# Kernel tuning notes

Measured on AMD Instinct MI355X. Metric: run time of the kernel, lower is better.

The kernel has to match this reference:

```python
import jax, jax.numpy as jnp
import numpy as np

HEADS = 8


def setup_inputs() -> dict:
    key = jax.random.key(0)
    ks = jax.random.split(key, 18)
    B, L, D, N = 512, 70, 128, 100000
    r = lambda i, shape: jax.random.normal(ks[i], shape, dtype=jnp.float32) * 0.1
    return {
        "hidden": r(0, (B, L, D)),
        "hidden0": r(1, (B, L, D)),
        "mask": jnp.ones((B, L), dtype=jnp.int32),
        "s": r(2, (B, D)),
        "emb": r(3, (N, D)),
        "attn_in_w": r(4, (3 * D, D)),
        "attn_in_b": r(5, (3 * D,)),
        "attn_out_w": r(6, (D, D)),
        "attn_out_b": r(7, (D,)),
        "w_zero": r(8, (D, D)),
        "b_zero": r(9, (D,)),
        "w_one": r(10, (D, D)),
        "b_one": r(11, (D,)),
        "w_two": r(12, (D, D)),
        "b_two": r(13, (D,)),
        "w_three": r(14, (HEADS, D)),
        "w_gate": r(15, (1, 2 * D)),
        "w_trans": r(16, (D, 2 * D)),
        "b_trans": r(17, (D,)),
    }


def _mha(q, k, v, in_w, in_b, out_w, out_b, h):
    # torch.nn.MultiheadAttention, eval mode (dropout=0)
    B, Lq, D = q.shape
    Lk = k.shape[1]
    hd = D // h
    wq, wk, wv = jnp.split(in_w, 3, axis=0)
    bq, bk, bv = jnp.split(in_b, 3)
    qp = (q @ wq.T + bq).reshape(B, Lq, h, hd)
    kp = (k @ wk.T + bk).reshape(B, Lk, h, hd)
    vp = (v @ wv.T + bv).reshape(B, Lk, h, hd)
    scores = jnp.einsum("bqhd,bkhd->bhqk", qp, kp) / jnp.sqrt(jnp.float32(hd))
    w = jax.nn.softmax(scores, axis=-1)
    o = jnp.einsum("bhqk,bkhd->bqhd", w, vp).reshape(B, Lq, D)
    return o @ out_w.T + out_b


def reference(hidden, hidden0, mask, s, emb,
              attn_in_w, attn_in_b, attn_out_w, attn_out_b,
              w_zero, b_zero, w_one, b_one, w_two, b_two,
              w_three, w_gate, w_trans, b_trans):
    B, L, D = hidden.shape
    H = HEADS
    # last-item gather (last_k = 1)
    last_idx = jnp.clip(jnp.sum(mask, axis=1) - 1, 0, 1000)
    ht0 = hidden[jnp.arange(B), last_idx]  # [B, D]
    ht1 = ht0
    # attention of pooled session vector over item states
    ht = _mha(s[:, None, :], hidden, hidden,
              attn_in_w, attn_in_b, attn_out_w, attn_out_b, H)  # [B, 1, D]
    # sigmoid gated fusion of hidden0 / hidden
    sigma = jax.nn.sigmoid(jnp.concatenate([hidden0, hidden], axis=-1) @ w_gate.T)  # [B, L, 1]
    hidden = hidden0 * sigma + hidden * (1.0 - sigma)
    # additive multi-head attention scores
    q0 = (ht1 @ w_zero.T + b_zero)[:, None, :]          # [B, 1, D]
    q1 = ht @ w_one.T + b_one                           # [B, 1, D]
    q2 = hidden @ w_two.T + b_two                       # [B, L, D]
    alpha = jax.nn.sigmoid(q1 + q2 + q0) @ w_three.T    # [B, L, H]
    alpha = jnp.where((mask == 0)[:, :, None], -jnp.inf, alpha)
    alpha = jax.nn.softmax(alpha, axis=1)
    # head-split mask-weighted sum reduction
    mf = mask.astype(hidden.dtype)[:, :, None]
    a = jnp.sum((alpha[..., None] * hidden.reshape(B, L, H, D // H)).reshape(B, L, D) * mf, axis=1)  # [B, D]
    # hybrid transform with last item
    a = jnp.concatenate([a, ht0], axis=1) @ w_trans.T + b_trans
    # normalized scoring against item table (skipping padding idx 0)
    b = emb[1:]
    a = a / (jnp.linalg.norm(a, axis=1, keepdims=True) + 1e-12)
    b = b / (jnp.linalg.norm(b, axis=1, keepdims=True) + 1e-12)
    scores = 12.0 * (a @ b.T)  # [B, n_node-1]
    return scores
```

## Files before the change

kernel.cpp:

```cpp
#include <hip/hip_runtime.h>
#include <hip/hip_bf16.h>

#define B_SZ 512
#define L_SZ 70
#define D_SZ 128
#define NCOL 99999
#define M_ROWS (B_SZ * L_SZ)

typedef __attribute__((ext_vector_type(4))) float f32x4;
typedef __attribute__((ext_vector_type(8))) short bf16x8;
typedef __attribute__((ext_vector_type(4))) short s16x4;
typedef __attribute__((ext_vector_type(8))) unsigned short u16x8;

static __device__ __forceinline__ short f2bf(float x) {
    union { float f; unsigned u; } v; v.f = x;
    unsigned r = v.u + 0x7fffu + ((v.u >> 16) & 1u);
    return (short)(r >> 16);
}
static __device__ __forceinline__ float bf2f(unsigned short h) {
    union { unsigned u; float f; } v; v.u = ((unsigned)h) << 16; return v.f;
}

__global__ void k_prep(const float* attn_in_w, const float* w_two,
                       const float* attn_out_w, const float* w_zero,
                       const float* w_one, const float* w_trans,
                       short* Wkv, short* W2,
                       float* wqT, float* woT, float* w0T, float* w1T, float* wtT) {
    int i = blockIdx.x * 256 + threadIdx.x;
    if (i < 256 * 128) Wkv[i] = f2bf(attn_in_w[128 * 128 + i]);
    if (i < 128 * 128) {
        W2[i] = f2bf(w_two[i]);
        int r = i >> 7, c = i & 127;
        wqT[c * 128 + r] = attn_in_w[i];
        woT[c * 128 + r] = attn_out_w[i];
        w0T[c * 128 + r] = w_zero[i];
        w1T[c * 128 + r] = w_one[i];
    }
    if (i < 128 * 256) {
        int r = i >> 8, c = i & 255;
        wtT[c * 128 + r] = w_trans[i];
    }
}

__global__ void k_gatekv(const float* hidden, const float* hidden0, const float* w_gate,
                         const short* Wkv, const float* attn_in_b,
                         short* g_bf, short* kv) {
    __shared__ float wg[256];
    __shared__ short h_lds[64][136];
    int t = threadIdx.x;
    int r0 = blockIdx.x * 64;
    wg[t] = w_gate[t];
    int row = t >> 2, q = t & 3;
    const float* hrow  = hidden  + (size_t)(r0 + row) * 128;
    const float* h0row = hidden0 + (size_t)(r0 + row) * 128;
    float h[32], h0[32];
    for (int i = 0; i < 8; i++) {
        float4 a = *(const float4*)(hrow  + i * 16 + q * 4);
        float4 b = *(const float4*)(h0row + i * 16 + q * 4);
        h[i*4+0]=a.x; h[i*4+1]=a.y; h[i*4+2]=a.z; h[i*4+3]=a.w;
        h0[i*4+0]=b.x; h0[i*4+1]=b.y; h0[i*4+2]=b.z; h0[i*4+3]=b.w;
    }
    __syncthreads();
    float p = 0.f;
    for (int i = 0; i < 8; i++)
        for (int j = 0; j < 4; j++) {
            int c = i * 16 + q * 4 + j;
            p += h0[i*4+j] * wg[c] + h[i*4+j] * wg[128 + c];
        }
    p += __shfl_xor(p, 1);
    p += __shfl_xor(p, 2);
    float sg = 1.f / (1.f + __expf(-p));
    float om = 1.f - sg;
    for (int i = 0; i < 8; i++) {
        s16x4 gv, hv;
        for (int j = 0; j < 4; j++) {
            gv[j] = f2bf(h0[i*4+j] * sg + h[i*4+j] * om);
            hv[j] = f2bf(h[i*4+j]);
        }
        int c = i * 16 + q * 4;
        *(s16x4*)(g_bf + (size_t)(r0 + row) * 128 + c) = gv;
        *(s16x4*)(&h_lds[row][c]) = hv;
    }
    __syncthreads();
    int lane = t & 63, w = t >> 6;
    int arl = lane & 15, kg = lane >> 4;
    int kbase = kg * 8;
    bf16x8 aF[4];
    for (int kk = 0; kk < 4; kk++)
        aF[kk] = *(const bf16x8*)(&h_lds[w * 16 + arl][kbase + kk * 32]);
    int cl = lane & 15;
    int rowbase = r0 + w * 16 + kg * 4;
    for (int ct = 0; ct < 16; ct++) {
        int c = ct * 16 + cl;
        f32x4 acc = {0.f, 0.f, 0.f, 0.f};
        const short* Brow = Wkv + c * 128 + kbase;
        for (int kk = 0; kk < 4; kk++) {
            bf16x8 bF = *(const bf16x8*)(Brow + kk * 32);
            acc = __builtin_amdgcn_mfma_f32_16x16x32_bf16(aF[kk], bF, acc, 0, 0, 0);
        }
        float bias = attn_in_b[128 + c];
        for (int rg = 0; rg < 4; rg++)
            kv[(size_t)(rowbase + rg) * 256 + c] = f2bf(acc[rg] + bias);
    }
}

__global__ void k_attn(const float* hidden, const int* mask, const float* s,
                       const float* wqT, const float* attn_in_b,
                       const short* kv,
                       const float* woT, const float* attn_out_b,
                       const float* w0T, const float* b_zero,
                       const float* w1T, const float* b_one,
                       float* ht0, float* q01) {
    int b = blockIdx.x, t = threadIdx.x;
    __shared__ unsigned short kp_s[L_SZ][136];
    __shared__ float s_sh[128], qp_s[128], o_s[128], ht_s[128], ht0_s[128];
    __shared__ float sc[8][72];
    __shared__ int idx_sh;
    if (t < 64) {
        int acc = 0;
        for (int l = t; l < L_SZ; l += 64) acc += mask[b * L_SZ + l];
        for (int off = 32; off; off >>= 1) acc += __shfl_down(acc, off);
        if (t == 0) {
            int idx = acc - 1;
            if (idx < 0) idx = 0;
            if (idx > L_SZ - 1) idx = L_SZ - 1;
            idx_sh = idx;
        }
    }
    s_sh[t] = s[b * 128 + t];
    const unsigned short* kvrow = (const unsigned short*)kv + (size_t)b * L_SZ * 256;
    for (int i = t; i < L_SZ * 128; i += 128) {
        int l = i >> 7, d = i & 127;
        kp_s[l][d] = kvrow[l * 256 + d];
    }
    __syncthreads();
    {
        float h0 = hidden[((size_t)b * L_SZ + idx_sh) * 128 + t];
        ht0[b * 128 + t] = h0;
        ht0_s[t] = h0;
        float acc = attn_in_b[t];
        for (int k = 0; k < 128; k++) acc += s_sh[k] * wqT[k * 128 + t];
        qp_s[t] = acc;
    }
    __syncthreads();
    for (int task = t; task < 8 * L_SZ; task += 128) {
        int h = task / L_SZ, l = task - (task / L_SZ) * L_SZ;
        const u16x8* kp = (const u16x8*)&kp_s[l][h * 16];
        u16x8 k0 = kp[0], k1 = kp[1];
        float acc = 0.f;
        for (int j = 0; j < 8; j++)
            acc += qp_s[h * 16 + j] * bf2f(k0[j]) + qp_s[h * 16 + 8 + j] * bf2f(k1[j]);
        sc[h][l] = acc * 0.25f;
    }
    __syncthreads();
    if (t < 8) {
        float m = -1e30f;
        for (int l = 0; l < L_SZ; l++) m = fmaxf(m, sc[t][l]);
        float ssum = 0.f;
        for (int l = 0; l < L_SZ; l++) { float e = __expf(sc[t][l] - m); sc[t][l] = e; ssum += e; }
        float inv = 1.f / ssum;
        for (int l = 0; l < L_SZ; l++) sc[t][l] *= inv;
    }
    __syncthreads();
    {
        int h = t >> 4;
        float acc = 0.f;
        for (int l = 0; l < L_SZ; l++) acc += sc[h][l] * bf2f(kvrow[l * 256 + 128 + t]);
        o_s[t] = acc;
    }
    __syncthreads();
    {
        float acc = attn_out_b[t];
        for (int k = 0; k < 128; k++) acc += o_s[k] * woT[k * 128 + t];
        ht_s[t] = acc;
    }
    __syncthreads();
    {
        float acc = b_one[t] + b_zero[t];
        for (int k = 0; k < 128; k++) acc += ht_s[k] * w1T[k * 128 + t] + ht0_s[k] * w0T[k * 128 + t];
        q01[b * 128 + t] = acc;
    }
}

__global__ void k_gemm_q2_alpha(const short* g_bf, const short* W2, const float* b_two,
                                const float* q01, const float* w_three, float* alphaL) {
    int lane = threadIdx.x & 63, w = threadIdx.x >> 6;
    int r0 = blockIdx.x * 64 + w * 16;
    int ar = r0 + (lane & 15);
    int kbase = (lane >> 4) * 8;
    bf16x8 aF[4];
    const short* Arow = g_bf + ar * 128 + kbase;
    for (int kk = 0; kk < 4; kk++) aF[kk] = *(const bf16x8*)(Arow + kk * 32);
    float part[4][8];
    for (int r = 0; r < 4; r++)
        for (int h = 0; h < 8; h++) part[r][h] = 0.f;
    int cl = lane & 15;
    int rowbase = r0 + (lane >> 4) * 4;
    for (int ct = 0; ct < 8; ct++) {
        int c = ct * 16 + cl;
        f32x4 acc = {0.f, 0.f, 0.f, 0.f};
        const short* Brow = W2 + c * 128 + kbase;
        for (int kk = 0; kk < 4; kk++) {
            bf16x8 bF = *(const bf16x8*)(Brow + kk * 32);
            acc = __builtin_amdgcn_mfma_f32_16x16x32_bf16(aF[kk], bF, acc, 0, 0, 0);
        }
        float bias = b_two[c];
        for (int rg = 0; rg < 4; rg++) {
            int row = rowbase + rg;
            int bb = row / L_SZ;
            float val = acc[rg] + bias + q01[bb * 128 + c];
            float sg = 1.f / (1.f + __expf(-val));
            for (int h = 0; h < 8; h++) part[rg][h] += sg * w_three[h * 128 + c];
        }
    }
    for (int off = 1; off < 16; off <<= 1)
        for (int rg = 0; rg < 4; rg++)
            for (int h = 0; h < 8; h++)
                part[rg][h] += __shfl_xor(part[rg][h], off);
    if ((lane & 15) == 0) {
        for (int rg = 0; rg < 4; rg++) {
            int row = rowbase + rg;
            for (int h = 0; h < 8; h++) alphaL[row * 8 + h] = part[rg][h];
        }
    }
}

__global__ void k_alpha_a(const float* alphaL, const int* mask, const short* g_bf,
                          const float* ht0, const float* wtT, const float* b_trans,
                          short* a_bf) {
    int b = blockIdx.x, t = threadIdx.x;
    __shared__ float aw[L_SZ][8];
    __shared__ float mf[L_SZ];
    __shared__ float a_s[128];
    __shared__ float ht0_s[128];
    __shared__ float red[2];
    for (int i = t; i < L_SZ; i += 128) mf[i] = (float)mask[b * L_SZ + i];
    for (int i = t; i < L_SZ * 8; i += 128) aw[i >> 3][i & 7] = alphaL[b * L_SZ * 8 + i];
    ht0_s[t] = ht0[b * 128 + t];
    __syncthreads();
    if (t < 8) {
        float m = -1e30f;
        for (int l = 0; l < L_SZ; l++) {
            float v = (mf[l] == 0.f) ? -1e30f : aw[l][t];
            if (v > m) m = v;
        }
        float ssum = 0.f;
        for (int l = 0; l < L_SZ; l++) {
            float v = (mf[l] == 0.f) ? -1e30f : aw[l][t];
            float e = __expf(v - m);
            ssum += e; aw[l][t] = e;
        }
        float inv = 1.f / ssum;
        for (int l = 0; l < L_SZ; l++) aw[l][t] *= inv;
    }
    __syncthreads();
    int h = t >> 4;
    float acc = 0.f;
    const unsigned short* grow = (const unsigned short*)g_bf + b * L_SZ * 128 + t;
    for (int l = 0; l < L_SZ; l++) acc += aw[l][h] * bf2f(grow[l * 128]) * mf[l];
    a_s[t] = acc;
    __syncthreads();
    float a2 = b_trans[t];
    for (int k = 0; k < 128; k++)
        a2 += a_s[k] * wtT[k * 128 + t] + ht0_s[k] * wtT[(128 + k) * 128 + t];
    float sq = a2 * a2;
    for (int off = 32; off; off >>= 1) sq += __shfl_down(sq, off);
    if ((t & 63) == 0) red[t >> 6] = sq;
    __syncthreads();
    float nrm = sqrtf(red[0] + red[1]) + 1e-12f;
    a_bf[b * 128 + t] = f2bf(a2 / nrm);
}

__global__ void __launch_bounds__(256, 4) k_final(const short* a_bf, const float* emb, float* out) {
    __shared__ float cbuf[4][16][36];
    int t = threadIdx.x;
    int lane = t & 63, w = t >> 6;
    int bx = blockIdx.x;
    int cl = lane & 15, kg = lane >> 4;
    int kbase = kg * 8;

    bf16x8 bF[2][4];
    for (int ct2 = 0; ct2 < 2; ct2++) {
        int c0 = bx * 128 + w * 32 + ct2 * 16 + cl;
        float x[4][8];
        float ss = 0.f;
        if (c0 < NCOL) {
            const float* e = emb + (size_t)(c0 + 1) * 128 + kbase;
            for (int kk = 0; kk < 4; kk++) {
                float4 v0 = *(const float4*)(e + kk * 32);
                float4 v1 = *(const float4*)(e + kk * 32 + 4);
                x[kk][0] = v0.x; x[kk][1] = v0.y; x[kk][2] = v0.z; x[kk][3] = v0.w;
                x[kk][4] = v1.x; x[kk][5] = v1.y; x[kk][6] = v1.z; x[kk][7] = v1.w;
                for (int j = 0; j < 8; j++) ss += x[kk][j] * x[kk][j];
            }
        } else {
            for (int kk = 0; kk < 4; kk++)
                for (int j = 0; j < 8; j++) x[kk][j] = 0.f;
        }
        ss += __shfl_xor(ss, 16);
        ss += __shfl_xor(ss, 32);
        float inv = 1.f / (sqrtf(ss) + 1e-12f);
        for (int kk = 0; kk < 4; kk++) {
            bf16x8 f;
            for (int j = 0; j < 8; j++) f[j] = f2bf(x[kk][j] * inv);
            bF[ct2][kk] = f;
        }
    }

    int cend = NCOL - bx * 128;
    if (cend > 128) cend = 128;
    int srow = lane >> 2, schunk = lane & 3;
    int scb = w * 32 + schunk * 8;

    for (int rt = 0; rt < 32; rt++) {
        bf16x8 aF[4];
        const short* Arow = a_bf + (size_t)(rt * 16 + cl) * 128 + kbase;
        for (int kk = 0; kk < 4; kk++) aF[kk] = *(const bf16x8*)(Arow + kk * 32);
        f32x4 acc0 = {0.f, 0.f, 0.f, 0.f}, acc1 = {0.f, 0.f, 0.f, 0.f};
        for (int kk = 0; kk < 4; kk++) {
            acc0 = __builtin_amdgcn_mfma_f32_16x16x32_bf16(aF[kk], bF[0][kk], acc0, 0, 0, 0);
            acc1 = __builtin_amdgcn_mfma_f32_16x16x32_bf16(aF[kk], bF[1][kk], acc1, 0, 0, 0);
        }
        for (int rg = 0; rg < 4; rg++) {
            cbuf[w][kg * 4 + rg][cl]      = 12.f * acc0[rg];
            cbuf[w][kg * 4 + rg][16 + cl] = 12.f * acc1[rg];
        }
        asm volatile("s_waitcnt lgkmcnt(0)" ::: "memory");
        f32x4 v0 = *(const f32x4*)&cbuf[w][srow][schunk * 8];
        f32x4 v1 = *(const f32x4*)&cbuf[w][srow][schunk * 8 + 4];
        asm volatile("s_waitcnt lgkmcnt(0)" ::: "memory");
        size_t gr = (size_t)(rt * 16 + srow) * NCOL + (size_t)bx * 128 + scb;
        if (scb + 7 < cend) {
            *(f32x4*)(out + gr) = v0;
            *(f32x4*)(out + gr + 4) = v1;
        } else {
            for (int j = 0; j < 4; j++) if (scb + j < cend) out[gr + j] = v0[j];
            for (int j = 0; j < 4; j++) if (scb + 4 + j < cend) out[gr + 4 + j] = v1[j];
        }
    }
}

extern "C" void kernel_launch(void* const* d_in, const int* in_sizes, int n_in,
                              void* d_out, int out_size, void* d_ws, size_t ws_size,
                              hipStream_t stream) {
    const float* hidden     = (const float*)d_in[0];
    const float* hidden0    = (const float*)d_in[1];
    const int*   mask       = (const int*)d_in[2];
    const float* s          = (const float*)d_in[3];
    const float* emb        = (const float*)d_in[4];
    const float* attn_in_w  = (const float*)d_in[5];
    const float* attn_in_b  = (const float*)d_in[6];
    const float* attn_out_w = (const float*)d_in[7];
    const float* attn_out_b = (const float*)d_in[8];
    const float* w_zero     = (const float*)d_in[9];
    const float* b_zero     = (const float*)d_in[10];
    const float* w_one      = (const float*)d_in[11];
    const float* b_one      = (const float*)d_in[12];
    const float* w_two      = (const float*)d_in[13];
    const float* b_two      = (const float*)d_in[14];
    const float* w_three    = (const float*)d_in[15];
    const float* w_gate     = (const float*)d_in[16];
    const float* w_trans    = (const float*)d_in[17];
    const float* b_trans    = (const float*)d_in[18];
    float* out = (float*)d_out;

    char* p = (char*)d_ws;
    float* ht0    = (float*)p; p += (size_t)B_SZ * 128 * 4;
    float* q01    = (float*)p; p += (size_t)B_SZ * 128 * 4;
    float* alphaL = (float*)p; p += (size_t)B_SZ * L_SZ * 8 * 4;
    short* a_bf   = (short*)p; p += (size_t)B_SZ * 128 * 2;
    short* Wkv    = (short*)p; p += (size_t)256 * 128 * 2;
    short* W2     = (short*)p; p += (size_t)128 * 128 * 2;
    float* wqT    = (float*)p; p += (size_t)128 * 128 * 4;
    float* woT    = (float*)p; p += (size_t)128 * 128 * 4;
    float* w0T    = (float*)p; p += (size_t)128 * 128 * 4;
    float* w1T    = (float*)p; p += (size_t)128 * 128 * 4;
    float* wtT    = (float*)p; p += (size_t)256 * 128 * 4;
    short* g_bf   = (short*)p; p += (size_t)M_ROWS * 128 * 2;
    short* kv     = (short*)p; p += (size_t)M_ROWS * 256 * 2;

    k_prep<<<128, 256, 0, stream>>>(attn_in_w, w_two, attn_out_w, w_zero, w_one, w_trans,
                                    Wkv, W2, wqT, woT, w0T, w1T, wtT);
    k_gatekv<<<M_ROWS / 64, 256, 0, stream>>>(hidden, hidden0, w_gate, Wkv, attn_in_b,
                                              g_bf, kv);
    k_attn<<<B_SZ, 128, 0, stream>>>(hidden, mask, s, wqT, attn_in_b, kv,
                                     woT, attn_out_b, w0T, b_zero, w1T, b_one, ht0, q01);
    k_gemm_q2_alpha<<<M_ROWS / 64, 256, 0, stream>>>(g_bf, W2, b_two, q01, w_three, alphaL);
    k_alpha_a<<<B_SZ, 128, 0, stream>>>(alphaL, mask, g_bf, ht0, wtT, b_trans, a_bf);
    k_final<<<(NCOL + 127) / 128, 256, 0, stream>>>(a_bf, emb, out);
}
```

Before: 462.2 us.

## Fuse gating, attention, alpha and transform into one per-batch kernel

Merges the gate/KV, attention, q2-alpha and alpha-reduction kernels into a single kernel with one block per batch row, keeping hidden and gated hidden in LDS as bf16. It also folds the K and V projections algebraically into the single query: the query is pushed through Wk so scores come straight from hidden, and the per-head weighted hidden sum is projected by Wv afterwards. This avoids materialising and rereading the large K/V and gated-hidden intermediates and cuts several launches. In exchange there are only 512 blocks, each with heavy LDS use and long serial phases, which may limit occupancy.

```diff
diff --git a/kernel.cpp b/kernel.cpp
--- a/kernel.cpp
+++ b/kernel.cpp
@@ -5,7 +5,7 @@
 #define L_SZ 70
 #define D_SZ 128
 #define NCOL 99999
-#define M_ROWS (B_SZ * L_SZ)
+#define HPAD 152
 
 typedef __attribute__((ext_vector_type(4))) float f32x4;
 typedef __attribute__((ext_vector_type(8))) short bf16x8;
@@ -24,14 +24,14 @@
 __global__ void k_prep(const float* attn_in_w, const float* w_two,
                        const float* attn_out_w, const float* w_zero,
                        const float* w_one, const float* w_trans,
-                       short* Wkv, short* W2,
-                       float* wqT, float* woT, float* w0T, float* w1T, float* wtT) {
+                       short* W2, float* wqT, float* woT, float* w0T,
+                       float* w1T, float* wvT, float* wtT) {
     int i = blockIdx.x * 256 + threadIdx.x;
-    if (i < 256 * 128) Wkv[i] = f2bf(attn_in_w[128 * 128 + i]);
     if (i < 128 * 128) {
         W2[i] = f2bf(w_two[i]);
         int r = i >> 7, c = i & 127;
         wqT[c * 128 + r] = attn_in_w[i];
+        wvT[c * 128 + r] = attn_in_w[(256 + r) * 128 + c];
         woT[c * 128 + r] = attn_out_w[i];
         w0T[c * 128 + r] = w_zero[i];
         w1T[c * 128 + r] = w_one[i];
@@ -42,233 +42,265 @@
     }
 }
 
-__global__ void k_gatekv(const float* hidden, const float* hidden0, const float* w_gate,
-                         const short* Wkv, const float* attn_in_b,
-                         short* g_bf, short* kv) {
-    __shared__ float wg[256];
-    __shared__ short h_lds[64][136];
-    int t = threadIdx.x;
-    int r0 = blockIdx.x * 64;
-    wg[t] = w_gate[t];
-    int row = t >> 2, q = t & 3;
-    const float* hrow  = hidden  + (size_t)(r0 + row) * 128;
-    const float* h0row = hidden0 + (size_t)(r0 + row) * 128;
-    float h[32], h0[32];
-    for (int i = 0; i < 8; i++) {
-        float4 a = *(const float4*)(hrow  + i * 16 + q * 4);
-        float4 b = *(const float4*)(h0row + i * 16 + q * 4);
-        h[i*4+0]=a.x; h[i*4+1]=a.y; h[i*4+2]=a.z; h[i*4+3]=a.w;
-        h0[i*4+0]=b.x; h0[i*4+1]=b.y; h0[i*4+2]=b.z; h0[i*4+3]=b.w;
-    }
-    __syncthreads();
-    float p = 0.f;
-    for (int i = 0; i < 8; i++)
-        for (int j = 0; j < 4; j++) {
-            int c = i * 16 + q * 4 + j;
-            p += h0[i*4+j] * wg[c] + h[i*4+j] * wg[128 + c];
-        }
-    p += __shfl_xor(p, 1);
-    p += __shfl_xor(p, 2);
-    float sg = 1.f / (1.f + __expf(-p));
-    float om = 1.f - sg;
-    for (int i = 0; i < 8; i++) {
-        s16x4 gv, hv;
-        for (int j = 0; j < 4; j++) {
-            gv[j] = f2bf(h0[i*4+j] * sg + h[i*4+j] * om);
-            hv[j] = f2bf(h[i*4+j]);
-        }
-        int c = i * 16 + q * 4;
-        *(s16x4*)(g_bf + (size_t)(r0 + row) * 128 + c) = gv;
-        *(s16x4*)(&h_lds[row][c]) = hv;
-    }
-    __syncthreads();
+__global__ void __launch_bounds__(256, 2)
+k_mega(const float* hidden, const float* hidden0, const int* mask, const float* s,
+       const float* attn_in_w, const float* attn_in_b, const float* attn_out_b,
+       const float* b_zero, const float* b_one,
+       const short* W2, const float* b_two, const float* w_three,
+       const float* w_gate,
+       const float* wqT, const float* woT, const float* w0T, const float* w1T,
+       const float* wvT, const float* wtT, const float* b_trans,
+       short* a_bf) {
+    int b = blockIdx.x, t = threadIdx.x;
     int lane = t & 63, w = t >> 6;
-    int arl = lane & 15, kg = lane >> 4;
-    int kbase = kg * 8;
-    bf16x8 aF[4];
-    for (int kk = 0; kk < 4; kk++)
-        aF[kk] = *(const bf16x8*)(&h_lds[w * 16 + arl][kbase + kk * 32]);
-    int cl = lane & 15;
-    int rowbase = r0 + w * 16 + kg * 4;
-    for (int ct = 0; ct < 16; ct++) {
-        int c = ct * 16 + cl;
-        f32x4 acc = {0.f, 0.f, 0.f, 0.f};
-        const short* Brow = Wkv + c * 128 + kbase;
-        for (int kk = 0; kk < 4; kk++) {
-            bf16x8 bF = *(const bf16x8*)(Brow + kk * 32);
-            acc = __builtin_amdgcn_mfma_f32_16x16x32_bf16(aF[kk], bF, acc, 0, 0, 0);
-        }
-        float bias = attn_in_b[128 + c];
-        for (int rg = 0; rg < 4; rg++)
-            kv[(size_t)(rowbase + rg) * 256 + c] = f2bf(acc[rg] + bias);
-    }
-}
-
-__global__ void k_attn(const float* hidden, const int* mask, const float* s,
-                       const float* wqT, const float* attn_in_b,
-                       const short* kv,
-                       const float* woT, const float* attn_out_b,
-                       const float* w0T, const float* b_zero,
-                       const float* w1T, const float* b_one,
-                       float* ht0, float* q01) {
-    int b = blockIdx.x, t = threadIdx.x;
-    __shared__ unsigned short kp_s[L_SZ][136];
-    __shared__ float s_sh[128], qp_s[128], o_s[128], ht_s[128], ht0_s[128];
-    __shared__ float sc[8][72];
+
+    __shared__ short h_lds[80][HPAD];
+    __shared__ short g_lds[80][HPAD];
+    __shared__ float zp[8][128];
+    __shared__ float sc_al[80][8];
+    __shared__ float wg_sh[256];
+    __shared__ float bufA[128];
+    __shared__ float bufB[128];
+    __shared__ float ht0_f[128], q01_s[128];
+    __shared__ float ch[8], mf[80], red[2];
     __shared__ int idx_sh;
-    if (t < 64) {
+
+    wg_sh[t] = w_gate[t];
+    if (t >= 128) bufA[t - 128] = s[(size_t)b * 128 + (t - 128)];
+    if (t < 70) mf[t] = (float)mask[b * L_SZ + t];
+    for (int i = t; i < 10 * HPAD; i += 256) g_lds[70 + i / HPAD][i % HPAD] = 0;
+    __syncthreads();
+
+    for (int lb = 0; lb < L_SZ; lb += 64) {
+        int l = lb + (t >> 2), q = t & 3;
+        if (l < L_SZ) {
+            const float* hr  = hidden  + ((size_t)b * L_SZ + l) * 128 + q * 32;
+            const float* h0r = hidden0 + ((size_t)b * L_SZ + l) * 128 + q * 32;
+            float4 hv4[8], h0v4[8];
+            for (int i = 0; i < 8; i++) {
+                hv4[i]  = *(const float4*)(hr  + i * 4);
+                h0v4[i] = *(const float4*)(h0r + i * 4);
+            }
+            float p = 0.f;
+            for (int i = 0; i < 8; i++) {
+                const float* hp = (const float*)&hv4[i];
+                const float* h0p = (const float*)&h0v4[i];
+                for (int j = 0; j < 4; j++) {
+                    int c = q * 32 + i * 4 + j;
+                    p += h0p[j] * wg_sh[c] + hp[j] * wg_sh[128 + c];
+                }
+            }
+            p += __shfl_xor(p, 1);
+            p += __shfl_xor(p, 2);
+            float sg = 1.f / (1.f + __expf(-p)), om = 1.f - sg;
+            for (int i = 0; i < 8; i++) {
+                const float* hp = (const float*)&hv4[i];
+                const float* h0p = (const float*)&h0v4[i];
+                s16x4 hv, gv;
+                for (int j = 0; j < 4; j++) {
+                    hv[j] = f2bf(hp[j]);
+                    gv[j] = f2bf(h0p[j] * sg + hp[j] * om);
+                }
+                int c = q * 32 + i * 4;
+                *(s16x4*)(&h_lds[l][c]) = hv;
+                *(s16x4*)(&g_lds[l][c]) = gv;
+            }
+        }
+    }
+    if (t == 0) {
         int acc = 0;
-        for (int l = t; l < L_SZ; l += 64) acc += mask[b * L_SZ + l];
-        for (int off = 32; off; off >>= 1) acc += __shfl_down(acc, off);
-        if (t == 0) {
-            int idx = acc - 1;
-            if (idx < 0) idx = 0;
-            if (idx > L_SZ - 1) idx = L_SZ - 1;
-            idx_sh = idx;
-        }
-    }
-    s_sh[t] = s[b * 128 + t];
-    const unsigned short* kvrow = (const unsigned short*)kv + (size_t)b * L_SZ * 256;
-    for (int i = t; i < L_SZ * 128; i += 128) {
-        int l = i >> 7, d = i & 127;
-        kp_s[l][d] = kvrow[l * 256 + d];
-    }
-    __syncthreads();
-    {
+        for (int l = 0; l < L_SZ; l++) acc += (int)mf[l];
+        int idx = acc - 1;
+        if (idx < 0) idx = 0;
+        if (idx > L_SZ - 1) idx = L_SZ - 1;
+        idx_sh = idx;
+    }
+    __syncthreads();
+
+    if (t < 128) {
         float h0 = hidden[((size_t)b * L_SZ + idx_sh) * 128 + t];
-        ht0[b * 128 + t] = h0;
-        ht0_s[t] = h0;
-        float acc = attn_in_b[t];
-        for (int k = 0; k < 128; k++) acc += s_sh[k] * wqT[k * 128 + t];
-        qp_s[t] = acc;
-    }
-    __syncthreads();
-    for (int task = t; task < 8 * L_SZ; task += 128) {
-        int h = task / L_SZ, l = task - (task / L_SZ) * L_SZ;
-        const u16x8* kp = (const u16x8*)&kp_s[l][h * 16];
-        u16x8 k0 = kp[0], k1 = kp[1];
-        float acc = 0.f;
-        for (int j = 0; j < 8; j++)
-            acc += qp_s[h * 16 + j] * bf2f(k0[j]) + qp_s[h * 16 + 8 + j] * bf2f(k1[j]);
-        sc[h][l] = acc * 0.25f;
-    }
-    __syncthreads();
+        ht0_f[t] = h0;
+        float a0 = 0, a1 = 0, a2 = 0, a3 = 0;
+        for (int k = 0; k < 128; k += 4) {
+            a0 += bufA[k] * wqT[k * 128 + t];
+            a1 += bufA[k + 1] * wqT[(k + 1) * 128 + t];
+            a2 += bufA[k + 2] * wqT[(k + 2) * 128 + t];
+            a3 += bufA[k + 3] * wqT[(k + 3) * 128 + t];
+        }
+        bufB[t] = attn_in_b[t] + ((a0 + a1) + (a2 + a3));
+    }
+    __syncthreads();
+
+    for (int out = t; out < 1024; out += 256) {
+        int h = out >> 7, d = out & 127;
+        const float* wk = attn_in_w + (size_t)(128 + h * 16) * 128 + d;
+        float a0 = 0, a1 = 0;
+        for (int j = 0; j < 16; j += 2) {
+            a0 += wk[j * 128] * bufB[h * 16 + j];
+            a1 += wk[(j + 1) * 128] * bufB[h * 16 + j + 1];
+        }
+        zp[h][d] = a0 + a1;
+    }
+    if (t < 8) {
+        float a = 0;
+        for (int j = 0; j < 16; j++) a += bufB[t * 16 + j] * attn_in_b[128 + t * 16 + j];
+        ch[t] = 0.25f * a;
+    }
+    __syncthreads();
+
+    for (int task = t; task < 8 * L_SZ; task += 256) {
+        int l = task % L_SZ, h = task / L_SZ;
+        const u16x8* hp = (const u16x8*)&h_lds[l][0];
+        float a0 = 0, a1 = 0, a2 = 0, a3 = 0;
+        for (int c = 0; c < 16; c += 2) {
+            u16x8 v0 = hp[c], v1 = hp[c + 1];
+            for (int j = 0; j < 8; j += 2) {
+                a0 += bf2f(v0[j]) * zp[h][c * 8 + j];
+                a1 += bf2f(v0[j + 1]) * zp[h][c * 8 + j + 1];
+                a2 += bf2f(v1[j]) * zp[h][c * 8 + 8 + j];
+                a3 += bf2f(v1[j + 1]) * zp[h][c * 8 + 8 + j + 1];
+            }
+        }
+        sc_al[l][h] = ((a0 + a1) + (a2 + a3)) * 0.25f + ch[h];
+    }
+    __syncthreads();
+
     if (t < 8) {
         float m = -1e30f;
-        for (int l = 0; l < L_SZ; l++) m = fmaxf(m, sc[t][l]);
-        float ssum = 0.f;
-        for (int l = 0; l < L_SZ; l++) { float e = __expf(sc[t][l] - m); sc[t][l] = e; ssum += e; }
-        float inv = 1.f / ssum;
-        for (int l = 0; l < L_SZ; l++) sc[t][l] *= inv;
-    }
-    __syncthreads();
+        for (int l = 0; l < L_SZ; l++) m = fmaxf(m, sc_al[l][t]);
+        float ss = 0.f;
+        for (int l = 0; l < L_SZ; l++) { float e = __expf(sc_al[l][t] - m); sc_al[l][t] = e; ss += e; }
+        float inv = 1.f / ss;
+        for (int l = 0; l < L_SZ; l++) sc_al[l][t] *= inv;
+    }
+    __syncthreads();
+
+    for (int out = t; out < 1024; out += 256) {
+        int h = out >> 7, d = out & 127;
+        float a0 = 0, a1 = 0;
+        for (int l = 0; l < L_SZ; l += 2) {
+            a0 += sc_al[l][h] * bf2f((unsigned short)h_lds[l][d]);
+            a1 += sc_al[l + 1][h] * bf2f((unsigned short)h_lds[l + 1][d]);
+        }
+        zp[h][d] = a0 + a1;
+    }
+    __syncthreads();
+
+    if (t < 128) {
+        int h = t >> 4;
+        float a0 = 0, a1 = 0, a2 = 0, a3 = 0;
+        for (int d = 0; d < 128; d += 4) {
+            a0 += wvT[d * 128 + t] * zp[h][d];
+            a1 += wvT[(d + 1) * 128 + t] * zp[h][d + 1];
+            a2 += wvT[(d + 2) * 128 + t] * zp[h][d + 2];
+            a3 += wvT[(d + 3) * 128 + t] * zp[h][d + 3];
+        }
+        bufA[t] = attn_in_b[256 + t] + ((a0 + a1) + (a2 + a3));
+    }
+    __syncthreads();
+
+    if (t < 128) {
+        float a0 = 0, a1 = 0, a2 = 0, a3 = 0;
+        for (int k = 0; k < 128; k += 4) {
+            a0 += bufA[k] * woT[k * 128 + t];
+            a1 += bufA[k + 1] * woT[(k + 1) * 128 + t];
+            a2 += bufA[k + 2] * woT[(k + 2) * 128 + t];
+            a3 += bufA[k + 3] * woT[(k + 3) * 128 + t];
+        }
+        bufB[t] = attn_out_b[t] + ((a0 + a1) + (a2 + a3));
+    }
+    __syncthreads();
+    if (t < 128) {
+        float a0 = 0, a1 = 0;
+        for (int k = 0; k < 128; k += 2) {
+            a0 += bufB[k] * w1T[k * 128 + t] + ht0_f[k] * w0T[k * 128 + t];
+            a1 += bufB[k + 1] * w1T[(k + 1) * 128 + t] + ht0_f[k + 1] * w0T[(k + 1) * 128 + t];
+        }
+        q01_s[t] = b_one[t] + b_zero[t] + a0 + a1;
+    }
+    __syncthreads();
+
     {
-        int h = t >> 4;
-        float acc = 0.f;
-        for (int l = 0; l < L_SZ; l++) acc += sc[h][l] * bf2f(kvrow[l * 256 + 128 + t]);
-        o_s[t] = acc;
-    }
-    __syncthreads();
-    {
-        float acc = attn_out_b[t];
-        for (int k = 0; k < 128; k++) acc += o_s[k] * woT[k * 128 + t];
-        ht_s[t] = acc;
-    }
-    __syncthreads();
-    {
-        float acc = b_one[t] + b_zero[t];
-        for (int k = 0; k < 128; k++) acc += ht_s[k] * w1T[k * 128 + t] + ht0_s[k] * w0T[k * 128 + t];
-        q01[b * 128 + t] = acc;
-    }
-}
-
-__global__ void k_gemm_q2_alpha(const short* g_bf, const short* W2, const float* b_two,
-                                const float* q01, const float* w_three, float* alphaL) {
-    int lane = threadIdx.x & 63, w = threadIdx.x >> 6;
-    int r0 = blockIdx.x * 64 + w * 16;
-    int ar = r0 + (lane & 15);
-    int kbase = (lane >> 4) * 8;
-    bf16x8 aF[4];
-    const short* Arow = g_bf + ar * 128 + kbase;
-    for (int kk = 0; kk < 4; kk++) aF[kk] = *(const bf16x8*)(Arow + kk * 32);
-    float part[4][8];
-    for (int r = 0; r < 4; r++)
-        for (int h = 0; h < 8; h++) part[r][h] = 0.f;
-    int cl = lane & 15;
-    int rowbase = r0 + (lane >> 4) * 4;
-    for (int ct = 0; ct < 8; ct++) {
-        int c = ct * 16 + cl;
-        f32x4 acc = {0.f, 0.f, 0.f, 0.f};
-        const short* Brow = W2 + c * 128 + kbase;
-        for (int kk = 0; kk < 4; kk++) {
-            bf16x8 bF = *(const bf16x8*)(Brow + kk * 32);
-            acc = __builtin_amdgcn_mfma_f32_16x16x32_bf16(aF[kk], bF, acc, 0, 0, 0);
-        }
-        float bias = b_two[c];
-        for (int rg = 0; rg < 4; rg++) {
-            int row = rowbase + rg;
-            int bb = row / L_SZ;
-            float val = acc[rg] + bias + q01[bb * 128 + c];
-            float sg = 1.f / (1.f + __expf(-val));
-            for (int h = 0; h < 8; h++) part[rg][h] += sg * w_three[h * 128 + c];
-        }
-    }
-    for (int off = 1; off < 16; off <<= 1)
-        for (int rg = 0; rg < 4; rg++)
-            for (int h = 0; h < 8; h++)
-                part[rg][h] += __shfl_xor(part[rg][h], off);
-    if ((lane & 15) == 0) {
-        for (int rg = 0; rg < 4; rg++) {
-            int row = rowbase + rg;
-            for (int h = 0; h < 8; h++) alphaL[row * 8 + h] = part[rg][h];
-        }
-    }
-}
-
-__global__ void k_alpha_a(const float* alphaL, const int* mask, const short* g_bf,
-                          const float* ht0, const float* wtT, const float* b_trans,
-                          short* a_bf) {
-    int b = blockIdx.x, t = threadIdx.x;
-    __shared__ float aw[L_SZ][8];
-    __shared__ float mf[L_SZ];
-    __shared__ float a_s[128];
-    __shared__ float ht0_s[128];
-    __shared__ float red[2];
-    for (int i = t; i < L_SZ; i += 128) mf[i] = (float)mask[b * L_SZ + i];
-    for (int i = t; i < L_SZ * 8; i += 128) aw[i >> 3][i & 7] = alphaL[b * L_SZ * 8 + i];
-    ht0_s[t] = ht0[b * 128 + t];
-    __syncthreads();
+        int cl = lane & 15, kg = lane >> 4, kbase = kg * 8;
+        for (int tile = w; tile < 5; tile += 4) {
+            bf16x8 aF[4];
+            for (int kk = 0; kk < 4; kk++)
+                aF[kk] = *(const bf16x8*)(&g_lds[tile * 16 + cl][kbase + kk * 32]);
+            float part[4][8];
+            for (int r = 0; r < 4; r++)
+                for (int h = 0; h < 8; h++) part[r][h] = 0.f;
+            for (int ct = 0; ct < 8; ct++) {
+                int c = ct * 16 + cl;
+                f32x4 acc = {0.f, 0.f, 0.f, 0.f};
+                const short* Brow = W2 + c * 128 + kbase;
+                for (int kk = 0; kk < 4; kk++) {
+                    bf16x8 bF = *(const bf16x8*)(Brow + kk * 32);
+                    acc = __builtin_amdgcn_mfma_f32_16x16x32_bf16(aF[kk], bF, acc, 0, 0, 0);
+                }
+                float bias = b_two[c];
+                for (int rg = 0; rg < 4; rg++) {
+                    float val = acc[rg] + bias + q01_s[c];
+                    float sg = 1.f / (1.f + __expf(-val));
+                    for (int h = 0; h < 8; h++) part[rg][h] += sg * w_three[h * 128 + c];
+                }
+            }
+            for (int off = 1; off < 16; off <<= 1)
+                for (int rg = 0; rg < 4; rg++)
+                    for (int h = 0; h < 8; h++)
+                        part[rg][h] += __shfl_xor(part[rg][h], off);
+            if (cl == 0) {
+                for (int rg = 0; rg < 4; rg++)
+                    for (int h = 0; h < 8; h++)
+                        sc_al[tile * 16 + kg * 4 + rg][h] = part[rg][h];
+            }
+        }
+    }
+    __syncthreads();
+
     if (t < 8) {
         float m = -1e30f;
         for (int l = 0; l < L_SZ; l++) {
-            float v = (mf[l] == 0.f) ? -1e30f : aw[l][t];
+            float v = (mf[l] == 0.f) ? -1e30f : sc_al[l][t];
             if (v > m) m = v;
         }
-        float ssum = 0.f;
+        float ss = 0.f;
         for (int l = 0; l < L_SZ; l++) {
-            float v = (mf[l] == 0.f) ? -1e30f : aw[l][t];
+            float v = (mf[l] == 0.f) ? -1e30f : sc_al[l][t];
             float e = __expf(v - m);
-            ssum += e; aw[l][t] = e;
-        }
-        float inv = 1.f / ssum;
-        for (int l = 0; l < L_SZ; l++) aw[l][t] *= inv;
-    }
-    __syncthreads();
-    int h = t >> 4;
-    float acc = 0.f;
-    const unsigned short* grow = (const unsigned short*)g_bf + b * L_SZ * 128 + t;
-    for (int l = 0; l < L_SZ; l++) acc += aw[l][h] * bf2f(grow[l * 128]) * mf[l];
-    a_s[t] = acc;
-    __syncthreads();
-    float a2 = b_trans[t];
-    for (int k = 0; k < 128; k++)
-        a2 += a_s[k] * wtT[k * 128 + t] + ht0_s[k] * wtT[(128 + k) * 128 + t];
-    float sq = a2 * a2;
-    for (int off = 32; off; off >>= 1) sq += __shfl_down(sq, off);
-    if ((t & 63) == 0) red[t >> 6] = sq;
-    __syncthreads();
-    float nrm = sqrtf(red[0] + red[1]) + 1e-12f;
-    a_bf[b * 128 + t] = f2bf(a2 / nrm);
+            sc_al[l][t] = e; ss += e;
+        }
+        float inv = 1.f / ss;
+        for (int l = 0; l < L_SZ; l++) sc_al[l][t] *= inv;
+    }
+    __syncthreads();
+    if (t < 128) {
+        int h = t >> 4;
+        float a0 = 0, a1 = 0;
+        for (int l = 0; l < L_SZ; l += 2) {
+            a0 += sc_al[l][h] * bf2f((unsigned short)g_lds[l][t]) * mf[l];
+            a1 += sc_al[l + 1][h] * bf2f((unsigned short)g_lds[l + 1][t]) * mf[l + 1];
+        }
+        bufB[t] = a0 + a1;
+    }
+    __syncthreads();
+
+    float a2v = 0.f;
+    if (t < 128) {
+        float a0 = 0, a1 = 0;
+        for (int k = 0; k < 128; k += 2) {
+            a0 += bufB[k] * wtT[k * 128 + t] + ht0_f[k] * wtT[(128 + k) * 128 + t];
+            a1 += bufB[k + 1] * wtT[(k + 1) * 128 + t] + ht0_f[k + 1] * wtT[(129 + k) * 128 + t];
+        }
+        a2v = b_trans[t] + a0 + a1;
+        float sq = a2v * a2v;
+        for (int off = 32; off; off >>= 1) sq += __shfl_down(sq, off);
+        if (lane == 0) red[w] = sq;
+    }
+    __syncthreads();
+    if (t < 128) {
+        float nrm = sqrtf(red[0] + red[1]) + 1e-12f;
+        a_bf[b * 128 + t] = f2bf(a2v / nrm);
+    }
 }
 
 __global__ void __launch_bounds__(256, 4) k_final(const short* a_bf, const float* emb, float* out) {
@@ -365,27 +397,20 @@
     float* out = (float*)d_out;
 
     char* p = (char*)d_ws;
-    float* ht0    = (float*)p; p += (size_t)B_SZ * 128 * 4;
-    float* q01    = (float*)p; p += (size_t)B_SZ * 128 * 4;
-    float* alphaL = (float*)p; p += (size_t)B_SZ * L_SZ * 8 * 4;
-    short* a_bf   = (short*)p; p += (size_t)B_SZ * 128 * 2;
-    short* Wkv    = (short*)p; p += (size_t)256 * 128 * 2;
-    short* W2     = (short*)p; p += (size_t)128 * 128 * 2;
-    float* wqT    = (float*)p; p += (size_t)128 * 128 * 4;
-    float* woT    = (float*)p; p += (size_t)128 * 128 * 4;
-    float* w0T    = (float*)p; p += (size_t)128 * 128 * 4;
-    float* w1T    = (float*)p; p += (size_t)128 * 128 * 4;
-    float* wtT    = (float*)p; p += (size_t)256 * 128 * 4;
-    short* g_bf   = (short*)p; p += (size_t)M_ROWS * 128 * 2;
-    short* kv     = (short*)p; p += (size_t)M_ROWS * 256 * 2;
+    short* a_bf = (short*)p; p += (size_t)B_SZ * 128 * 2;
+    short* W2   = (short*)p; p += (size_t)128 * 128 * 2;
+    float* wqT  = (float*)p; p += (size_t)128 * 128 * 4;
+    float* woT  = (float*)p; p += (size_t)128 * 128 * 4;
+    float* w0T  = (float*)p; p += (size_t)128 * 128 * 4;
+    float* w1T  = (float*)p; p += (size_t)128 * 128 * 4;
+    float* wvT  = (float*)p; p += (size_t)128 * 128 * 4;
+    float* wtT  = (float*)p; p += (size_t)256 * 128 * 4;
 
     k_prep<<<128, 256, 0, stream>>>(attn_in_w, w_two, attn_out_w, w_zero, w_one, w_trans,
-                                    Wkv, W2, wqT, woT, w0T, w1T, wtT);
-    k_gatekv<<<M_ROWS / 64, 256, 0, stream>>>(hidden, hidden0, w_gate, Wkv, attn_in_b,
-                                              g_bf, kv);
-    k_attn<<<B_SZ, 128, 0, stream>>>(hidden, mask, s, wqT, attn_in_b, kv,
-                                     woT, attn_out_b, w0T, b_zero, w1T, b_one, ht0, q01);
-    k_gemm_q2_alpha<<<M_ROWS / 64, 256, 0, stream>>>(g_bf, W2, b_two, q01, w_three, alphaL);
-    k_alpha_a<<<B_SZ, 128, 0, stream>>>(alphaL, mask, g_bf, ht0, wtT, b_trans, a_bf);
+                                    W2, wqT, woT, w0T, w1T, wvT, wtT);
+    k_mega<<<B_SZ, 256, 0, stream>>>(hidden, hidden0, mask, s,
+                                     attn_in_w, attn_in_b, attn_out_b,
+                                     b_zero, b_one, W2, b_two, w_three, w_gate,
+                                     wqT, woT, w0T, w1T, wvT, wtT, b_trans, a_bf);
     k_final<<<(NCOL + 127) / 128, 256, 0, stream>>>(a_bf, emb, out);
 }
```

Result: faster. 437.8 us (-5.3%).
